# Performance work log

Measured on AMD Instinct MI355X. Metric: run time of the kernel, lower is better.

The kernel has to match this reference:

```python
import jax, jax.numpy as jnp
import numpy as np

N_NODES = 50000
N_EDGES = 400000
N_GRAPHS = 512
NF = 64      # node_features
EF = 32      # edge_features (RBF bins)
AIF = 92     # atom_input_features
FC = 128     # fc_features
L = 3        # conv layers
EPS = 1e-5   # BatchNorm eps


def _bn(x, gamma, beta):
    # BatchNorm1d, training-mode statistics over the batch (edge/node) dim
    m = x.mean(0)
    v = x.var(0)  # biased variance, matches torch normalization
    return (x - m) * jax.lax.rsqrt(v + EPS) * gamma + beta


def _rbf(d):
    # RBFExpansion(vmin=0, vmax=8, bins=EF): gamma = 1/mean(diff(centers))
    centers = jnp.linspace(0.0, 8.0, EF)
    gamma = 1.0 / (centers[1] - centers[0])
    return jnp.exp(-gamma * (d[:, None] - centers) ** 2)  # [E, EF]


def setup_inputs() -> dict:
    key = jax.random.key(0)
    ks = jax.random.split(key, 12)
    s = 0.05
    IN = 2 * NF + EF
    return {
        "atom_features": jax.random.normal(ks[0], (N_NODES, AIF), dtype=jnp.float32),
        "bondlength": jax.random.uniform(ks[1], (N_EDGES,), dtype=jnp.float32) * 8.0,
        "src": jax.random.randint(ks[2], (N_EDGES,), 0, N_NODES),
        "dst": jax.random.randint(ks[3], (N_EDGES,), 0, N_NODES),
        "graph_ids": jnp.sort(jax.random.randint(ks[4], (N_NODES,), 0, N_GRAPHS)),
        "W_emb": jax.random.normal(ks[5], (AIF, NF), dtype=jnp.float32) * s,
        "b_emb": jnp.zeros((NF,), jnp.float32),
        "Wi": jax.random.normal(ks[6], (L, IN, NF), dtype=jnp.float32) * s,
        "bi": jnp.zeros((L, NF), jnp.float32),
        "gi": jnp.ones((L, NF), jnp.float32),
        "bti": jnp.zeros((L, NF), jnp.float32),
        "Wu": jax.random.normal(ks[7], (L, IN, NF), dtype=jnp.float32) * s,
        "bu": jnp.zeros((L, NF), jnp.float32),
        "gu": jnp.ones((L, NF), jnp.float32),
        "btu": jnp.zeros((L, NF), jnp.float32),
        "g_bn": jnp.ones((L, NF), jnp.float32),
        "b_bn": jnp.zeros((L, NF), jnp.float32),
        "W_fc": jax.random.normal(ks[8], (NF, FC), dtype=jnp.float32) * s,
        "b_fc": jnp.zeros((FC,), jnp.float32),
        "W_out": jax.random.normal(ks[9], (FC, 1), dtype=jnp.float32) * s,
        "b_out": jnp.zeros((1,), jnp.float32),
    }


def reference(atom_features, bondlength, src, dst, graph_ids,
              W_emb, b_emb, Wi, bi, gi, bti, Wu, bu, gu, btu,
              g_bn, b_bn, W_fc, b_fc, W_out, b_out):
    e = _rbf(bondlength)                       # [E, EF]
    h = atom_features @ W_emb + b_emb          # [N, NF]
    for l in range(L):
        # gather + concat: [E, 2*NF + EF]
        z = jnp.concatenate([h[src], h[dst], e], axis=1)
        gate = jax.nn.sigmoid(_bn(z @ Wi[l] + bi[l], gi[l], bti[l]))
        upd = jax.nn.softplus(_bn(z @ Wu[l] + bu[l], gu[l], btu[l]))
        msg = gate * upd                       # [E, NF]
        agg = jax.ops.segment_sum(msg, dst, num_segments=N_NODES)
        h = jax.nn.softplus(h + _bn(agg, g_bn[l], b_bn[l]))
    # AvgPooling over nodes per graph
    counts = jax.ops.segment_sum(jnp.ones((N_NODES, 1), h.dtype), graph_ids,
                                 num_segments=N_GRAPHS)
    pooled = jax.ops.segment_sum(h, graph_ids, num_segments=N_GRAPHS)
    pooled = pooled / jnp.maximum(counts, 1.0)  # [G, NF]
    f = jax.nn.softplus(pooled)
    f = jax.nn.softplus(f @ W_fc + b_fc)
    f = jax.nn.softplus(f)
    out = f @ W_out + b_out                    # [G, 1]
    return jnp.squeeze(out)                    # [G]
```

## Files before the change

kernel.cpp:

```cpp
#include <hip/hip_runtime.h>
#include <math.h>

#define N_NODES 50000
#define N_EDGES 400000
#define N_GRAPHS 512
#define TBL 2048
#define EPSBN 1e-5f

__device__ __forceinline__ float softplusf(float x) {
  return fmaxf(x, 0.0f) + log1pf(expf(-fabsf(x)));
}
__device__ __forceinline__ float sigmoidf(float x) {
  return 1.0f / (1.0f + expf(-x));
}
__device__ __forceinline__ void fma4(float4& acc, float s, const float4& w) {
  acc.x = fmaf(s, w.x, acc.x);
  acc.y = fmaf(s, w.y, acc.y);
  acc.z = fmaf(s, w.z, acc.z);
  acc.w = fmaf(s, w.w, acc.w);
}

__global__ void k_emb(const float* __restrict__ atom,
                      const float* __restrict__ Wemb,
                      const float* __restrict__ bemb,
                      float* __restrict__ h) {
  __shared__ float sW[92 * 64];
  __shared__ float sA[32 * 92];
  const int tid = threadIdx.x;
  for (int i = tid; i < 92 * 64; i += 256) sW[i] = Wemb[i];

  const int t0 = blockIdx.x * 32;
  const int nt = min(32, N_NODES - t0);
  {
    const float* srcp = atom + (size_t)t0 * 92;
    const int tot = nt * 92;
    for (int i = tid; i < tot; i += 256) sA[i] = srcp[i];
  }
  __syncthreads();

  const int col = tid & 63;
  const int ng = tid >> 6;
  const float bb = bemb[col];
  float acc[8];
#pragma unroll
  for (int i = 0; i < 8; ++i) acc[i] = bb;

  for (int kc = 0; kc < 92; kc += 4) {
    const float w0 = sW[(kc + 0) * 64 + col];
    const float w1 = sW[(kc + 1) * 64 + col];
    const float w2 = sW[(kc + 2) * 64 + col];
    const float w3 = sW[(kc + 3) * 64 + col];
#pragma unroll
    for (int i = 0; i < 8; ++i) {
      const float4 a = *(const float4*)&sA[(ng * 8 + i) * 92 + kc];
      acc[i] = fmaf(a.x, w0, acc[i]);
      acc[i] = fmaf(a.y, w1, acc[i]);
      acc[i] = fmaf(a.z, w2, acc[i]);
      acc[i] = fmaf(a.w, w3, acc[i]);
    }
  }
#pragma unroll
  for (int i = 0; i < 8; ++i) {
    const int n = t0 + ng * 8 + i;
    if (n < N_NODES) h[(size_t)n * 64 + col] = acc[i];
  }
}

__global__ void k_pq(const float* __restrict__ h,
                     const float* __restrict__ Wi_l,
                     const float* __restrict__ Wu_l,
                     float* __restrict__ PA,
                     float* __restrict__ PB) {
  __shared__ float sWA[64 * 128];
  __shared__ float sWB[64 * 128];
  __shared__ float sH[32 * 64];
  const int tid = threadIdx.x;

  for (int i = tid; i < 64 * 64; i += 256) {
    const int k = i >> 6, c = i & 63;
    sWA[k * 128 + c]      = Wi_l[k * 64 + c];
    sWA[k * 128 + 64 + c] = Wu_l[k * 64 + c];
    sWB[k * 128 + c]      = Wi_l[(64 + k) * 64 + c];
    sWB[k * 128 + 64 + c] = Wu_l[(64 + k) * 64 + c];
  }
  const int t0 = blockIdx.x * 32;
  const int nt = min(32, N_NODES - t0);
  {
    const float4* srcp = (const float4*)(h + (size_t)t0 * 64);
    const int tot4 = nt * 16;
    float4* dstp = (float4*)sH;
    for (int i = tid; i < tot4; i += 256) dstp[i] = srcp[i];
  }
  __syncthreads();

  const int wave = tid >> 6, lane = tid & 63;
  const float* wcol = (lane < 32) ? (sWA + 4 * lane) : (sWB + 4 * (lane - 32));
  const int jj = (lane < 32) ? 4 * lane : 4 * (lane - 32);
  float* OUTb = (lane < 32) ? PA : PB;

  float4 acc[8];
#pragma unroll
  for (int i = 0; i < 8; ++i) acc[i] = make_float4(0.f, 0.f, 0.f, 0.f);

  for (int kc = 0; kc < 64; kc += 4) {
    const float4 w0 = *(const float4*)(wcol + (kc + 0) * 128);
    const float4 w1 = *(const float4*)(wcol + (kc + 1) * 128);
    const float4 w2 = *(const float4*)(wcol + (kc + 2) * 128);
    const float4 w3 = *(const float4*)(wcol + (kc + 3) * 128);
#pragma unroll
    for (int i = 0; i < 8; ++i) {
      const float4 a = *(const float4*)&sH[(wave * 8 + i) * 64 + kc];
      fma4(acc[i], a.x, w0);
      fma4(acc[i], a.y, w1);
      fma4(acc[i], a.z, w2);
      fma4(acc[i], a.w, w3);
    }
  }
#pragma unroll
  for (int i = 0; i < 8; ++i) {
    const int n = t0 + wave * 8 + i;
    if (n < N_NODES) *(float4*)&OUTb[(size_t)n * 128 + jj] = acc[i];
  }
}

__global__ void k_tbl(const float* __restrict__ Wi_l,
                      const float* __restrict__ Wu_l,
                      float* __restrict__ tbl) {
  const int wave = threadIdx.x >> 6, lane = threadIdx.x & 63;
  const int t = blockIdx.x * (blockDim.x >> 6) + wave;
  if (t >= TBL) return;
  const float d = 8.0f * (float)t / (float)(TBL - 1);
  float gi_ = 0.f, gu_ = 0.f;
#pragma unroll
  for (int k = 0; k < 32; ++k) {
    const float c = 8.0f * (float)k / 31.0f;
    const float dd = d - c;
    const float r = expf(-3.875f * dd * dd);
    gi_ = fmaf(r, Wi_l[(128 + k) * 64 + lane], gi_);
    gu_ = fmaf(r, Wu_l[(128 + k) * 64 + lane], gu_);
  }
  tbl[(size_t)t * 128 + lane] = gi_;
  tbl[(size_t)t * 128 + 64 + lane] = gu_;
}

__device__ __forceinline__ void edge_pre(int e, int lane,
                                         const int* __restrict__ src,
                                         const int* __restrict__ dst,
                                         const float* __restrict__ bond,
                                         const float* __restrict__ PA,
                                         const float* __restrict__ PB,
                                         const float* __restrict__ tbl,
                                         float& yg, float& yu, int& dnode) {
  const int s = src[e];
  const int d2 = dst[e];
  const float d = bond[e];
  float f = d * ((float)(TBL - 1) / 8.0f);
  f = fminf(fmaxf(f, 0.0f), (float)(TBL - 1));
  int i0 = (int)f;
  if (i0 > TBL - 2) i0 = TBL - 2;
  const float fr = f - (float)i0;
  const float* ta = tbl + (size_t)i0 * 128 + lane;
  const float rg = fmaf(fr, ta[128] - ta[0], ta[0]);
  const float ru = fmaf(fr, ta[192] - ta[64], ta[64]);
  const float* pa = PA + (size_t)s * 128 + lane;
  const float* pb = PB + (size_t)d2 * 128 + lane;
  yg = pa[0] + pb[0] + rg;
  yu = pa[64] + pb[64] + ru;
  dnode = d2;
}

__global__ void k_edge_stats(const int* __restrict__ src,
                             const int* __restrict__ dst,
                             const float* __restrict__ bond,
                             const float* __restrict__ PA,
                             const float* __restrict__ PB,
                             const float* __restrict__ tbl,
                             float* __restrict__ stats) {
  const int wave = threadIdx.x >> 6, lane = threadIdx.x & 63;
  const int wpb = blockDim.x >> 6;
  const int nw = wpb * gridDim.x;
  float sg = 0.f, qg = 0.f, su = 0.f, qu = 0.f;
  for (int e = blockIdx.x * wpb + wave; e < N_EDGES; e += nw) {
    float yg, yu; int dn;
    edge_pre(e, lane, src, dst, bond, PA, PB, tbl, yg, yu, dn);
    sg += yg; qg = fmaf(yg, yg, qg);
    su += yu; qu = fmaf(yu, yu, qu);
  }
  __shared__ float red[4][4][64];
  red[0][wave][lane] = sg;
  red[1][wave][lane] = qg;
  red[2][wave][lane] = su;
  red[3][wave][lane] = qu;
  __syncthreads();
  const float v = red[wave][0][lane] + red[wave][1][lane] +
                  red[wave][2][lane] + red[wave][3][lane];
  atomicAdd(&stats[wave * 64 + lane], v);
}

__global__ void k_fin_gu(const float* __restrict__ stats,
                         const float* __restrict__ gi_l, const float* __restrict__ bti_l,
                         const float* __restrict__ gu_l, const float* __restrict__ btu_l,
                         float* __restrict__ coefs) {
  const int j = threadIdx.x;
  const float invE = 1.0f / (float)N_EDGES;
  float m = stats[j] * invE;
  float v = stats[64 + j] * invE - m * m;
  float a = gi_l[j] * rsqrtf(v + EPSBN);
  coefs[j] = a;
  coefs[64 + j] = fmaf(-m, a, bti_l[j]);
  m = stats[128 + j] * invE;
  v = stats[192 + j] * invE - m * m;
  a = gu_l[j] * rsqrtf(v + EPSBN);
  coefs[128 + j] = a;
  coefs[192 + j] = fmaf(-m, a, btu_l[j]);
}

__global__ void k_edge_apply(const int* __restrict__ src,
                             const int* __restrict__ dst,
                             const float* __restrict__ bond,
                             const float* __restrict__ PA,
                             const float* __restrict__ PB,
                             const float* __restrict__ tbl,
                             const float* __restrict__ coefs,
                             float* __restrict__ agg) {
  const int wave = threadIdx.x >> 6, lane = threadIdx.x & 63;
  const int wpb = blockDim.x >> 6;
  const int nw = wpb * gridDim.x;
  const float ag = coefs[lane], bg = coefs[64 + lane];
  const float au = coefs[128 + lane], bu = coefs[192 + lane];
  for (int e = blockIdx.x * wpb + wave; e < N_EDGES; e += nw) {
    float yg, yu; int dn;
    edge_pre(e, lane, src, dst, bond, PA, PB, tbl, yg, yu, dn);
    const float gate = sigmoidf(fmaf(ag, yg, bg));
    const float upd = softplusf(fmaf(au, yu, bu));
    atomicAdd(&agg[(size_t)dn * 64 + lane], gate * upd);
  }
}

__global__ void k_agg_stats(const float* __restrict__ agg, float* __restrict__ stats) {
  const int wave = threadIdx.x >> 6, lane = threadIdx.x & 63;
  const int wpb = blockDim.x >> 6;
  const int nw = wpb * gridDim.x;
  float s = 0.f, q = 0.f;
  for (int n = blockIdx.x * wpb + wave; n < N_NODES; n += nw) {
    const float v = agg[(size_t)n * 64 + lane];
    s += v; q = fmaf(v, v, q);
  }
  __shared__ float red[2][4][64];
  red[0][wave][lane] = s;
  red[1][wave][lane] = q;
  __syncthreads();
  if (wave < 2) {
    const float v = red[wave][0][lane] + red[wave][1][lane] +
                    red[wave][2][lane] + red[wave][3][lane];
    atomicAdd(&stats[256 + wave * 64 + lane], v);
  }
}

__global__ void k_fin_agg(const float* __restrict__ stats,
                          const float* __restrict__ gbn_l, const float* __restrict__ bbn_l,
                          float* __restrict__ coefs) {
  const int j = threadIdx.x;
  const float invN = 1.0f / (float)N_NODES;
  const float m = stats[256 + j] * invN;
  const float v = stats[320 + j] * invN - m * m;
  const float a = gbn_l[j] * rsqrtf(v + EPSBN);
  coefs[256 + j] = a;
  coefs[320 + j] = fmaf(-m, a, bbn_l[j]);
}

__global__ void k_hupd(float* __restrict__ h, const float* __restrict__ agg,
                       const float* __restrict__ coefs) {
  const int stride = blockDim.x * gridDim.x;
  for (int i = blockIdx.x * blockDim.x + threadIdx.x; i < N_NODES * 64; i += stride) {
    const int j = i & 63;
    const float x = h[i] + fmaf(coefs[256 + j], agg[i], coefs[320 + j]);
    h[i] = softplusf(x);
  }
}

__global__ void k_pool(const float* __restrict__ h, const int* __restrict__ gid,
                       float* __restrict__ pooled, float* __restrict__ counts) {
  const int wave = threadIdx.x >> 6, lane = threadIdx.x & 63;
  const int wpb = blockDim.x >> 6;
  const int nw = wpb * gridDim.x;
  for (int n = blockIdx.x * wpb + wave; n < N_NODES; n += nw) {
    const int g = gid[n];
    atomicAdd(&pooled[(size_t)g * 64 + lane], h[(size_t)n * 64 + lane]);
    if (lane == 0) atomicAdd(&counts[g], 1.0f);
  }
}

__global__ void k_final(const float* __restrict__ pooled, const float* __restrict__ counts,
                        const float* __restrict__ Wfc, const float* __restrict__ bfc,
                        const float* __restrict__ Wout, const float* __restrict__ bout,
                        float* __restrict__ out) {
  __shared__ float f1[64];
  __shared__ float red[128];
  const int g = blockIdx.x, t = threadIdx.x;
  if (t < 64) {
    const float c = fmaxf(counts[g], 1.0f);
    f1[t] = softplusf(pooled[(size_t)g * 64 + t] / c);
  }
  __syncthreads();
  float acc = bfc[t];
#pragma unroll
  for (int k = 0; k < 64; ++k) acc = fmaf(f1[k], Wfc[k * 128 + t], acc);
  red[t] = softplusf(softplusf(acc)) * Wout[t];
  __syncthreads();
  for (int s2 = 64; s2 > 0; s2 >>= 1) {
    if (t < s2) red[t] += red[t + s2];
    __syncthreads();
  }
  if (t == 0) out[g] = red[0] + bout[0];
}

extern "C" void kernel_launch(void* const* d_in, const int* in_sizes, int n_in,
                              void* d_out, int out_size, void* d_ws, size_t ws_size,
                              hipStream_t stream) {
  const float* atom = (const float*)d_in[0];
  const float* bond = (const float*)d_in[1];
  const int* src = (const int*)d_in[2];
  const int* dst = (const int*)d_in[3];
  const int* gid = (const int*)d_in[4];
  const float* Wemb = (const float*)d_in[5];
  const float* bemb = (const float*)d_in[6];
  const float* Wi = (const float*)d_in[7];
  const float* gi = (const float*)d_in[9];
  const float* bti = (const float*)d_in[10];
  const float* Wu = (const float*)d_in[11];
  const float* gub = (const float*)d_in[13];
  const float* btu = (const float*)d_in[14];
  const float* gbn = (const float*)d_in[15];
  const float* bbn = (const float*)d_in[16];
  const float* Wfc = (const float*)d_in[17];
  const float* bfc = (const float*)d_in[18];
  const float* Wout = (const float*)d_in[19];
  const float* bout = (const float*)d_in[20];

  float* h = (float*)d_ws;
  float* PA = h + (size_t)N_NODES * 64;
  float* PB = PA + (size_t)N_NODES * 128;
  float* agg = PB + (size_t)N_NODES * 128;
  float* tbl = agg + (size_t)N_NODES * 64;
  float* stats = tbl + (size_t)TBL * 128;
  float* coefs = stats + 384;
  float* pooled = coefs + 384;
  float* counts = pooled + (size_t)N_GRAPHS * 64;

  const int ntiles = (N_NODES + 31) / 32;

  k_emb<<<ntiles, 256, 0, stream>>>(atom, Wemb, bemb, h);
  for (int l = 0; l < 3; ++l) {
    const float* Wi_l = Wi + (size_t)l * 160 * 64;
    const float* Wu_l = Wu + (size_t)l * 160 * 64;
    (void)hipMemsetAsync(stats, 0, 384 * sizeof(float), stream);
    (void)hipMemsetAsync(agg, 0, (size_t)N_NODES * 64 * sizeof(float), stream);
    k_pq<<<ntiles, 256, 0, stream>>>(h, Wi_l, Wu_l, PA, PB);
    k_tbl<<<TBL / 4, 256, 0, stream>>>(Wi_l, Wu_l, tbl);
    k_edge_stats<<<2048, 256, 0, stream>>>(src, dst, bond, PA, PB, tbl, stats);
    k_fin_gu<<<1, 64, 0, stream>>>(stats, gi + l * 64, bti + l * 64,
                                   gub + l * 64, btu + l * 64, coefs);
    k_edge_apply<<<2048, 256, 0, stream>>>(src, dst, bond, PA, PB, tbl, coefs, agg);
    k_agg_stats<<<512, 256, 0, stream>>>(agg, stats);
    k_fin_agg<<<1, 64, 0, stream>>>(stats, gbn + l * 64, bbn + l * 64, coefs);
    k_hupd<<<1024, 256, 0, stream>>>(h, agg, coefs);
  }
  (void)hipMemsetAsync(pooled, 0, (size_t)(N_GRAPHS * 64 + N_GRAPHS) * sizeof(float), stream);
  k_pool<<<512, 256, 0, stream>>>(h, gid, pooled, counts);
  k_final<<<N_GRAPHS, 128, 0, stream>>>(pooled, counts, Wfc, bfc, Wout, bout,
                                        (float*)d_out);
}
```

Before: 1.783 ms.

## Build dst-sorted CSR once and aggregate edges per node without atomics

Builds a CSR grouping of edges by destination (degree count, scan, scatter) once before the layers. The edge stats and apply kernels then iterate per node, load the PB row once per node, and accumulate messages in registers. This removes the per-edge atomicAdd into agg, the agg memset and the separate agg-stats pass. Pooling also sums runs of sorted graph ids locally before issuing atomics. The CSR build adds one-time cost and a single-block scan, and per-node degree imbalance may leave some waves idle.

Measured after the change: 1.792 ms. Within noise of the previous version (+0.5%).

```diff
diff --git a/kernel.cpp b/kernel.cpp
--- a/kernel.cpp
+++ b/kernel.cpp
@@ -143,17 +143,63 @@
   tbl[(size_t)t * 128 + 64 + lane] = gu_;
 }
 
-__device__ __forceinline__ void edge_pre(int e, int lane,
-                                         const int* __restrict__ src,
-                                         const int* __restrict__ dst,
-                                         const float* __restrict__ bond,
+__global__ void k_deg(const int* __restrict__ dst, int* __restrict__ deg) {
+  const int stride = blockDim.x * gridDim.x;
+  for (int e = blockIdx.x * blockDim.x + threadIdx.x; e < N_EDGES; e += stride)
+    atomicAdd(&deg[dst[e]], 1);
+}
+
+__global__ void k_scan(const int* __restrict__ deg, int* __restrict__ offs,
+                       int* __restrict__ cursor) {
+  __shared__ int part[1024];
+  const int t = threadIdx.x;
+  const int CHUNK = (N_NODES + 1023) / 1024;
+  const int base = t * CHUNK;
+  int s = 0;
+  for (int i = 0; i < CHUNK; ++i) {
+    const int idx = base + i;
+    if (idx < N_NODES) s += deg[idx];
+  }
+  part[t] = s;
+  __syncthreads();
+  for (int off = 1; off < 1024; off <<= 1) {
+    int v = (t >= off) ? part[t - off] : 0;
+    __syncthreads();
+    part[t] += v;
+    __syncthreads();
+  }
+  int run = (t > 0) ? part[t - 1] : 0;
+  for (int i = 0; i < CHUNK; ++i) {
+    const int idx = base + i;
+    if (idx < N_NODES) {
+      offs[idx] = run;
+      cursor[idx] = run;
+      run += deg[idx];
+    }
+  }
+  if (t == 1023) offs[N_NODES] = run;
+}
+
+__global__ void k_scatter(const int* __restrict__ src, const int* __restrict__ dst,
+                          const float* __restrict__ bond,
+                          int* __restrict__ cursor,
+                          int* __restrict__ csr_src, float* __restrict__ csr_d) {
+  const int stride = blockDim.x * gridDim.x;
+  for (int e = blockIdx.x * blockDim.x + threadIdx.x; e < N_EDGES; e += stride) {
+    const int p = atomicAdd(&cursor[dst[e]], 1);
+    csr_src[p] = src[e];
+    csr_d[p] = bond[e];
+  }
+}
+
+__device__ __forceinline__ void csr_edge(int k, int lane,
+                                         const int* __restrict__ csr_src,
+                                         const float* __restrict__ csr_d,
                                          const float* __restrict__ PA,
-                                         const float* __restrict__ PB,
                                          const float* __restrict__ tbl,
-                                         float& yg, float& yu, int& dnode) {
-  const int s = src[e];
-  const int d2 = dst[e];
-  const float d = bond[e];
+                                         float& pg, float& pu) {
+  const int s = csr_src[k];
+  const float d = csr_d[k];
   float f = d * ((float)(TBL - 1) / 8.0f);
   f = fminf(fmaxf(f, 0.0f), (float)(TBL - 1));
   int i0 = (int)f;
@@ -163,28 +209,33 @@
   const float rg = fmaf(fr, ta[128] - ta[0], ta[0]);
   const float ru = fmaf(fr, ta[192] - ta[64], ta[64]);
   const float* pa = PA + (size_t)s * 128 + lane;
-  const float* pb = PB + (size_t)d2 * 128 + lane;
-  yg = pa[0] + pb[0] + rg;
-  yu = pa[64] + pb[64] + ru;
-  dnode = d2;
-}
-
-__global__ void k_edge_stats(const int* __restrict__ src,
-                             const int* __restrict__ dst,
-                             const float* __restrict__ bond,
-                             const float* __restrict__ PA,
-                             const float* __restrict__ PB,
-                             const float* __restrict__ tbl,
-                             float* __restrict__ stats) {
+  pg = pa[0] + rg;
+  pu = pa[64] + ru;
+}
+
+__global__ void k_stats_csr(const int* __restrict__ offs,
+                            const int* __restrict__ csr_src,
+                            const float* __restrict__ csr_d,
+                            const float* __restrict__ PA,
+                            const float* __restrict__ PB,
+                            const float* __restrict__ tbl,
+                            float* __restrict__ stats) {
   const int wave = threadIdx.x >> 6, lane = threadIdx.x & 63;
   const int wpb = blockDim.x >> 6;
   const int nw = wpb * gridDim.x;
   float sg = 0.f, qg = 0.f, su = 0.f, qu = 0.f;
-  for (int e = blockIdx.x * wpb + wave; e < N_EDGES; e += nw) {
-    float yg, yu; int dn;
-    edge_pre(e, lane, src, dst, bond, PA, PB, tbl, yg, yu, dn);
-    sg += yg; qg = fmaf(yg, yg, qg);
-    su += yu; qu = fmaf(yu, yu, qu);
+  for (int n = blockIdx.x * wpb + wave; n < N_NODES; n += nw) {
+    const float pbg = PB[(size_t)n * 128 + lane];
+    const float pbu = PB[(size_t)n * 128 + 64 + lane];
+    const int k0 = offs[n], k1 = offs[n + 1];
+    for (int k = k0; k < k1; ++k) {
+      float pg, pu;
+      csr_edge(k, lane, csr_src, csr_d, PA, tbl, pg, pu);
+      const float yg = pg + pbg;
+      const float yu = pu + pbu;
+      sg += yg; qg = fmaf(yg, yg, qg);
+      su += yu; qu = fmaf(yu, yu, qu);
+    }
   }
   __shared__ float red[4][4][64];
   red[0][wave][lane] = sg;
@@ -215,40 +266,40 @@
   coefs[192 + j] = fmaf(-m, a, btu_l[j]);
 }
 
-__global__ void k_edge_apply(const int* __restrict__ src,
-                             const int* __restrict__ dst,
-                             const float* __restrict__ bond,
-                             const float* __restrict__ PA,
-                             const float* __restrict__ PB,
-                             const float* __restrict__ tbl,
-                             const float* __restrict__ coefs,
-                             float* __restrict__ agg) {
+__global__ void k_apply_csr(const int* __restrict__ offs,
+                            const int* __restrict__ csr_src,
+                            const float* __restrict__ csr_d,
+                            const float* __restrict__ PA,
+                            const float* __restrict__ PB,
+                            const float* __restrict__ tbl,
+                            const float* __restrict__ coefs,
+                            float* __restrict__ agg,
+                            float* __restrict__ stats) {
   const int wave = threadIdx.x >> 6, lane = threadIdx.x & 63;
   const int wpb = blockDim.x >> 6;
   const int nw = wpb * gridDim.x;
   const float ag = coefs[lane], bg = coefs[64 + lane];
   const float au = coefs[128 + lane], bu = coefs[192 + lane];
-  for (int e = blockIdx.x * wpb + wave; e < N_EDGES; e += nw) {
-    float yg, yu; int dn;
-    edge_pre(e, lane, src, dst, bond, PA, PB, tbl, yg, yu, dn);
-    const float gate = sigmoidf(fmaf(ag, yg, bg));
-    const float upd = softplusf(fmaf(au, yu, bu));
-    atomicAdd(&agg[(size_t)dn * 64 + lane], gate * upd);
-  }
-}
-
-__global__ void k_agg_stats(const float* __restrict__ agg, float* __restrict__ stats) {
-  const int wave = threadIdx.x >> 6, lane = threadIdx.x & 63;
-  const int wpb = blockDim.x >> 6;
-  const int nw = wpb * gridDim.x;
-  float s = 0.f, q = 0.f;
+  float s2 = 0.f, q2 = 0.f;
   for (int n = blockIdx.x * wpb + wave; n < N_NODES; n += nw) {
-    const float v = agg[(size_t)n * 64 + lane];
-    s += v; q = fmaf(v, v, q);
+    const float pbg = PB[(size_t)n * 128 + lane];
+    const float pbu = PB[(size_t)n * 128 + 64 + lane];
+    const int k0 = offs[n], k1 = offs[n + 1];
+    float acc = 0.f;
+    for (int k = k0; k < k1; ++k) {
+      float pg, pu;
+      csr_edge(k, lane, csr_src, csr_d, PA, tbl, pg, pu);
+      const float gate = sigmoidf(fmaf(ag, pg + pbg, bg));
+      const float upd = softplusf(fmaf(au, pu + pbu, bu));
+      acc = fmaf(gate, upd, acc);
+    }
+    agg[(size_t)n * 64 + lane] = acc;
+    s2 += acc;
+    q2 = fmaf(acc, acc, q2);
   }
   __shared__ float red[2][4][64];
-  red[0][wave][lane] = s;
-  red[1][wave][lane] = q;
+  red[0][wave][lane] = s2;
+  red[1][wave][lane] = q2;
   __syncthreads();
   if (wave < 2) {
     const float v = red[wave][0][lane] + red[wave][1][lane] +
@@ -281,14 +332,27 @@
 
 __global__ void k_pool(const float* __restrict__ h, const int* __restrict__ gid,
                        float* __restrict__ pooled, float* __restrict__ counts) {
-  const int wave = threadIdx.x >> 6, lane = threadIdx.x & 63;
-  const int wpb = blockDim.x >> 6;
-  const int nw = wpb * gridDim.x;
-  for (int n = blockIdx.x * wpb + wave; n < N_NODES; n += nw) {
+  const int lane = threadIdx.x & 63;
+  const int wg = blockIdx.x * (blockDim.x >> 6) + (threadIdx.x >> 6);
+  const int nwaves = (blockDim.x >> 6) * gridDim.x;
+  const int chunk = (N_NODES + nwaves - 1) / nwaves;
+  const int n0 = wg * chunk;
+  if (n0 >= N_NODES) return;
+  const int n1 = min(n0 + chunk, N_NODES);
+  int cur = gid[n0];
+  float acc = 0.f, cnt = 0.f;
+  for (int n = n0; n < n1; ++n) {
     const int g = gid[n];
-    atomicAdd(&pooled[(size_t)g * 64 + lane], h[(size_t)n * 64 + lane]);
-    if (lane == 0) atomicAdd(&counts[g], 1.0f);
-  }
+    if (g != cur) {
+      atomicAdd(&pooled[(size_t)cur * 64 + lane], acc);
+      if (lane == 0) atomicAdd(&counts[cur], cnt);
+      cur = g; acc = 0.f; cnt = 0.f;
+    }
+    acc += h[(size_t)n * 64 + lane];
+    cnt += 1.0f;
+  }
+  atomicAdd(&pooled[(size_t)cur * 64 + lane], acc);
+  if (lane == 0) atomicAdd(&counts[cur], cnt);
 }
 
 __global__ void k_final(const float* __restrict__ pooled, const float* __restrict__ counts,
@@ -347,22 +411,31 @@
   float* coefs = stats + 384;
   float* pooled = coefs + 384;
   float* counts = pooled + (size_t)N_GRAPHS * 64;
+  int* deg = (int*)(counts + N_GRAPHS);
+  int* offs = deg + N_NODES;
+  int* cursor = offs + N_NODES + 1;
+  int* csr_src = cursor + N_NODES;
+  float* csr_d = (float*)(csr_src + N_EDGES);
 
   const int ntiles = (N_NODES + 31) / 32;
 
+  (void)hipMemsetAsync(deg, 0, (size_t)N_NODES * sizeof(int), stream);
   k_emb<<<ntiles, 256, 0, stream>>>(atom, Wemb, bemb, h);
+  k_deg<<<512, 256, 0, stream>>>(dst, deg);
+  k_scan<<<1, 1024, 0, stream>>>(deg, offs, cursor);
+  k_scatter<<<512, 256, 0, stream>>>(src, dst, bond, cursor, csr_src, csr_d);
+
   for (int l = 0; l < 3; ++l) {
     const float* Wi_l = Wi + (size_t)l * 160 * 64;
     const float* Wu_l = Wu + (size_t)l * 160 * 64;
     (void)hipMemsetAsync(stats, 0, 384 * sizeof(float), stream);
-    (void)hipMemsetAsync(agg, 0, (size_t)N_NODES * 64 * sizeof(float), stream);
     k_pq<<<ntiles, 256, 0, stream>>>(h, Wi_l, Wu_l, PA, PB);
     k_tbl<<<TBL / 4, 256, 0, stream>>>(Wi_l, Wu_l, tbl);
-    k_edge_stats<<<2048, 256, 0, stream>>>(src, dst, bond, PA, PB, tbl, stats);
+    k_stats_csr<<<2048, 256, 0, stream>>>(offs, csr_src, csr_d, PA, PB, tbl, stats);
     k_fin_gu<<<1, 64, 0, stream>>>(stats, gi + l * 64, bti + l * 64,
                                    gub + l * 64, btu + l * 64, coefs);
-    k_edge_apply<<<2048, 256, 0, stream>>>(src, dst, bond, PA, PB, tbl, coefs, agg);
-    k_agg_stats<<<512, 256, 0, stream>>>(agg, stats);
+    k_apply_csr<<<2048, 256, 0, stream>>>(offs, csr_src, csr_d, PA, PB, tbl,
+                                          coefs, agg, stats);
     k_fin_agg<<<1, 64, 0, stream>>>(stats, gbn + l * 64, bbn + l * 64, coefs);
     k_hupd<<<1024, 256, 0, stream>>>(h, agg, coefs);
   }
```
